# Kernel optimization log

Measured on AMD Instinct MI355X. Metric: run time of the kernel, lower is better.

## Reference

```python
import math
import jax, jax.numpy as jnp
import numpy as np

B, L, H, DH, DV = 4, 4096, 16, 128, 128
CHUNK = 1024
ROPE_BASE = 10000.0


def _rope_tables(length, dim, base, dtype):
    half = dim // 2
    freqs = jnp.exp(jnp.arange(half, dtype=jnp.float32) * (-(math.log(base) / half)))
    angles = jnp.arange(length, dtype=jnp.float32)[:, None] * freqs[None, :]  # (L, half)
    return jnp.cos(angles).astype(dtype), jnp.sin(angles).astype(dtype)


def _apply_rope(x, cos, sin):
    # x: (B, L, H, D); cos/sin: (L, D/2) -> broadcast (1, L, 1, D/2)
    half = x.shape[-1] // 2
    x1, x2 = x[..., :half], x[..., half:]
    c = cos[None, :, None, :]
    s = sin[None, :, None, :]
    return jnp.concatenate([x1 * c - x2 * s, x2 * c + x1 * s], axis=-1)


def setup_inputs() -> dict:
    key = jax.random.key(0)
    kq, kk, kv = jax.random.split(key, 3)
    q = jax.random.normal(kq, (B, L, H, DH), dtype=jnp.float32)
    k = jax.random.normal(kk, (B, L, H, DH), dtype=jnp.float32)
    v = jax.random.normal(kv, (B, L, H, DV), dtype=jnp.float32)
    return {"q": q, "k": k, "v": v}


def reference(q, k, v):
    b, l, h, dh = q.shape
    dv = v.shape[-1]
    n = l // CHUNK  # number of chunks

    cos, sin = _rope_tables(l, dh, ROPE_BASE, q.dtype)
    q = _apply_rope(q, cos, sin)
    k = _apply_rope(k, cos, sin)

    # Chunk-local causal attention: reshape to (B, N, H, C, D)
    qc = q.reshape(b, n, CHUNK, h, dh).transpose(0, 1, 3, 2, 4)
    kc = k.reshape(b, n, CHUNK, h, dh).transpose(0, 1, 3, 2, 4)
    vc = v.reshape(b, n, CHUNK, h, dv).transpose(0, 1, 3, 2, 4)

    scale = 1.0 / math.sqrt(dh)
    scores = jnp.einsum("bnhqd,bnhkd->bnhqk", qc, kc) * scale
    causal = jnp.tril(jnp.ones((CHUNK, CHUNK), dtype=bool))
    scores = jnp.where(causal[None, None, None], scores, jnp.finfo(scores.dtype).min)
    probs = jax.nn.softmax(scores, axis=-1)
    out = jnp.einsum("bnhqk,bnhkd->bnhqd", probs, vc)

    # back to (B, L, H, Dv)
    return out.transpose(0, 1, 3, 2, 4).reshape(b, l, h, dv)
```

## Files before the change

### kernel.cpp

```cpp
#include <hip/hip_runtime.h>
#include <math.h>
#include <stdint.h>


typedef __attribute__((ext_vector_type(8)))  short bf16x8;
typedef __attribute__((ext_vector_type(4)))  short bf16x4;
typedef __attribute__((ext_vector_type(16))) float f32x16;
typedef __attribute__((ext_vector_type(4)))  float f32x4;
typedef __attribute__((ext_vector_type(4)))  unsigned short us4;

__device__ __forceinline__ unsigned short f2bf(float x) {
  unsigned u = __float_as_uint(x);
  u += 0x7fff + ((u >> 16) & 1);
  return (unsigned short)(u >> 16);
}

__global__ __launch_bounds__(256) void rope_kernel(
    const float* __restrict__ q, const float* __restrict__ k,
    unsigned short* __restrict__ qws, unsigned short* __restrict__ kws)
{
  const int w    = threadIdx.x >> 6;
  const int lane = threadIdx.x & 63;
  const int r    = blockIdx.x * 4 + w;
  const int b    = r >> 16;
  const int rem  = r & 65535;
  const int l    = rem >> 4;
  const int h    = rem & 15;
  const float freq  = __builtin_amdgcn_exp2f((float)lane * -0.20762050593046014f);
  const float angle = (float)l * freq;
  float sn, cs;
  sincosf(angle, &sn, &cs);
  const size_t src = (size_t)r * 128 + lane;
  const int n = l >> 10, ck = l & 1023;
  const size_t dst = ((((size_t)b * 4 + n) * 16 + h) * 1024 + ck) * 128 + lane;
  const float QS = 0.12751741f;
  float x1 = q[src], x2 = q[src + 64];
  qws[dst]      = f2bf((x1 * cs - x2 * sn) * QS);
  qws[dst + 64] = f2bf((x2 * cs + x1 * sn) * QS);
  x1 = k[src]; x2 = k[src + 64];
  kws[dst]      = f2bf(x1 * cs - x2 * sn);
  kws[dst + 64] = f2bf(x2 * cs + x1 * sn);
}

__global__ __launch_bounds__(256) void vtrans_kernel(
    const float* __restrict__ v, unsigned short* __restrict__ vtws)
{
  __shared__ unsigned short tile[128 * 72];
  const int t   = threadIdx.x;
  const int ckb = blockIdx.x & 15;
  const int h   = (blockIdx.x >> 4) & 15;
  const int n   = (blockIdx.x >> 8) & 3;
  const int b   = blockIdx.x >> 10;
  const int i0  = (t >> 4) * 4;
  const int dv0 = (t & 15) * 8;
  const int l0  = n * 1024 + ckb * 64;
  const float* src = v + (((size_t)b * 4096 + l0) * 16 + h) * 128;
  unsigned short vals[4][8];
#pragma unroll
  for (int i = 0; i < 4; ++i) {
    const float* p = src + (size_t)(i0 + i) * 2048 + dv0;
    f32x4 a = *(const f32x4*)p;
    f32x4 c = *(const f32x4*)(p + 4);
#pragma unroll
    for (int jj = 0; jj < 4; ++jj) { vals[i][jj] = f2bf(a[jj]); vals[i][4 + jj] = f2bf(c[jj]); }
  }
#pragma unroll
  for (int dd = 0; dd < 8; ++dd) {
    us4 pk = { vals[0][dd], vals[1][dd], vals[2][dd], vals[3][dd] };
    *(us4*)&tile[(dv0 + dd) * 72 + i0] = pk;
  }
  __syncthreads();
  const int dv = t >> 1, hf = t & 1;
  const size_t dstb = ((((size_t)b * 4 + n) * 16 + h) * 128 + dv) * 1024 + ckb * 64 + hf * 32;
  const unsigned short* sl = &tile[dv * 72 + hf * 32];
#pragma unroll
  for (int kk = 0; kk < 4; ++kk)
    *(uint4*)(vtws + dstb + kk * 8) = *(const uint4*)(sl + kk * 8);
}

__global__ __launch_bounds__(256) void attn_kernel(
    const unsigned short* __restrict__ qws, const unsigned short* __restrict__ kws,
    const unsigned short* __restrict__ vtws, float* __restrict__ out)
{
  __shared__ unsigned short smem[64 * 136 + 128 * 72];
  unsigned short* kt = smem;
  unsigned short* vt = smem + 64 * 136;
  unsigned short* qstage = smem;

  const int qt   = blockIdx.x;
  const int nh   = blockIdx.y;
  const int b    = blockIdx.z;
  const int t    = threadIdx.x;
  const int lane = t & 63;
  const int w    = t >> 6;
  const int c    = lane & 31;
  const int g    = lane >> 5;

  const size_t bnh = (size_t)b * 64 + nh;
  const unsigned short* qbase = qws + bnh * (1024 * 128) + (size_t)qt * (128 * 128);
  const unsigned short* kbase = kws + bnh * (1024 * 128);
  const unsigned short* vbase = vtws + bnh * (128 * 1024);

#pragma unroll
  for (int it = 0; it < 8; ++it) {
    int u = it * 256 + t;
    int row = u >> 4, col = u & 15;
    uint4 val = ((const uint4*)qbase)[u];
    *(uint4*)((char*)qstage + row * 272 + col * 16) = val;
  }
  __syncthreads();
  const int qsub = w * 32;
  bf16x8 qf[8];
  {
    const char* qp = (const char*)qstage + (qsub + c) * 272 + g * 16;
#pragma unroll
    for (int f = 0; f < 8; ++f) qf[f] = *(const bf16x8*)(qp + f * 32);
  }
  __syncthreads();

  f32x16 acc[4] = {};
  float m_run = -INFINITY, l_run = 0.0f;
  const int q0w  = qt * 128 + qsub;
  const int rowq = q0w + c;
  const int jmax = 2 * qt + 2;

  for (int j = 0; j < jmax; ++j) {
    const uint4* kg = (const uint4*)(kbase + (size_t)j * (64 * 128));
#pragma unroll
    for (int it = 0; it < 4; ++it) {
      int u = it * 256 + t;
      int row = u >> 4, col = u & 15;
      uint4 val = kg[u];
      *(uint4*)((char*)kt + row * 272 + col * 16) = val;
    }
#pragma unroll
    for (int it = 0; it < 4; ++it) {
      int u = it * 256 + t;
      int dv = u >> 3, col = u & 7;
      uint4 val = *(const uint4*)(vbase + (size_t)dv * 1024 + j * 64 + col * 8);
      *(uint4*)((char*)vt + dv * 144 + col * 16) = val;
    }
    __syncthreads();

    const int kv0 = j * 64;
    if (kv0 <= q0w + 31) {
      f32x16 s[2];
#pragma unroll
      for (int ks = 0; ks < 2; ++ks) {
        f32x16 a = {};
        const char* kp = (const char*)kt + (ks * 32 + c) * 272 + g * 16;
#pragma unroll
        for (int f = 0; f < 8; ++f) {
          bf16x8 kf = *(const bf16x8*)(kp + f * 32);
          a = __builtin_amdgcn_mfma_f32_32x32x16_bf16(kf, qf[f], a, 0, 0, 0);
        }
        s[ks] = a;
      }
      const bool needmask = (kv0 + 63) > q0w;
      float mloc = -INFINITY;
      if (needmask) {
#pragma unroll
        for (int ks = 0; ks < 2; ++ks)
#pragma unroll
          for (int r = 0; r < 16; ++r) {
            int kv = kv0 + ks * 32 + (r & 3) + 8 * (r >> 2) + 4 * g;
            float val = (kv > rowq) ? -3.0e38f : s[ks][r];
            s[ks][r] = val;
            mloc = fmaxf(mloc, val);
          }
      } else {
#pragma unroll
        for (int ks = 0; ks < 2; ++ks)
#pragma unroll
          for (int r = 0; r < 16; ++r) mloc = fmaxf(mloc, s[ks][r]);
      }
      mloc = fmaxf(mloc, __shfl_xor(mloc, 32));
      const float mnew  = fmaxf(m_run, mloc);
      const float alpha = __builtin_amdgcn_exp2f(m_run - mnew);
      float rsum = 0.0f;
#pragma unroll
      for (int ks = 0; ks < 2; ++ks)
#pragma unroll
        for (int r = 0; r < 16; ++r) {
          float p = __builtin_amdgcn_exp2f(s[ks][r] - mnew);
          s[ks][r] = p;
          rsum += p;
        }
      rsum += __shfl_xor(rsum, 32);
      l_run = l_run * alpha + rsum;
      m_run = mnew;
#pragma unroll
      for (int d = 0; d < 4; ++d)
#pragma unroll
        for (int r = 0; r < 16; ++r) acc[d][r] *= alpha;
      bf16x4 pfr[8];
#pragma unroll
      for (int o = 0; o < 8; ++o) {
        const int ks = o >> 2, rb = 4 * (o & 3);
        unsigned u0 = __float_as_uint(s[ks][rb + 0]); u0 += 0x7fff + ((u0 >> 16) & 1);
        unsigned u1 = __float_as_uint(s[ks][rb + 1]); u1 += 0x7fff + ((u1 >> 16) & 1);
        unsigned u2 = __float_as_uint(s[ks][rb + 2]); u2 += 0x7fff + ((u2 >> 16) & 1);
        unsigned u3 = __float_as_uint(s[ks][rb + 3]); u3 += 0x7fff + ((u3 >> 16) & 1);
        union { unsigned uu[2]; bf16x4 bv; } pk;
        pk.uu[0] = __builtin_amdgcn_perm(u1, u0, 0x07060302u);
        pk.uu[1] = __builtin_amdgcn_perm(u3, u2, 0x07060302u);
        pfr[o] = pk.bv;
      }
      const char* vp = (const char*)vt + c * 144 + g * 8;
#pragma unroll
      for (int d = 0; d < 4; ++d) {
        f32x16 a = acc[d];
        const char* vpd = vp + d * 32 * 144;
#pragma unroll
        for (int o = 0; o < 8; ++o) {
          bf16x4 vf = *(const bf16x4*)(vpd + o * 16);
          a = __builtin_amdgcn_mfma_f32_32x32x8bf16_1k(vf, pfr[o], a, 0, 0, 0);
        }
        acc[d] = a;
      }
    }
    __syncthreads();
  }

  const float invl = 1.0f / l_run;
  const int n = nh >> 4, h = nh & 15;
  const size_t orow = (((size_t)b * 4096 + n * 1024 + rowq) * 16 + h) * 128;
#pragma unroll
  for (int d = 0; d < 4; ++d)
#pragma unroll
    for (int e = 0; e < 4; ++e) {
      f32x4 vv;
#pragma unroll
      for (int rr = 0; rr < 4; ++rr) vv[rr] = acc[d][4 * e + rr] * invl;
      *(f32x4*)(out + orow + 32 * d + 8 * e + 4 * g) = vv;
    }
}

extern "C" void kernel_launch(void* const* d_in, const int* in_sizes, int n_in,
                              void* d_out, int out_size, void* d_ws, size_t ws_size,
                              hipStream_t stream) {
  const float* q = (const float*)d_in[0];
  const float* k = (const float*)d_in[1];
  const float* v = (const float*)d_in[2];
  float* out = (float*)d_out;
  unsigned short* qws  = (unsigned short*)d_ws;
  unsigned short* kws  = qws + (size_t)33554432;
  unsigned short* vtws = kws + (size_t)33554432;

  rope_kernel<<<65536, 256, 0, stream>>>(q, k, qws, kws);
  vtrans_kernel<<<4096, 256, 0, stream>>>(v, vtws);
  attn_kernel<<<dim3(8, 64, 4), 256, 0, stream>>>(qws, kws, vtws, out);
}
```

Before: 609.5 us.

## Vectorize RoPE, prefetch K/V tiles into registers, skip redundant rescaling

The RoPE kernel now has each thread handle four elements, using vector loads and stores and hardware sin/cos on range-reduced revolutions instead of sincosf. The attention kernel prefetches the next K/V tile into registers while the current tile is being computed, which overlaps global loads with MFMA work. It also skips the accumulator rescale when no row's max changed, and swaps the grid order so blocks of the same query tile run together. The costs are higher register pressure and slightly lower sin/cos accuracy.

```diff
diff --git a/kernel.cpp b/kernel.cpp
--- a/kernel.cpp
+++ b/kernel.cpp
@@ -19,27 +19,38 @@
     const float* __restrict__ q, const float* __restrict__ k,
     unsigned short* __restrict__ qws, unsigned short* __restrict__ kws)
 {
-  const int w    = threadIdx.x >> 6;
-  const int lane = threadIdx.x & 63;
-  const int r    = blockIdx.x * 4 + w;
-  const int b    = r >> 16;
-  const int rem  = r & 65535;
-  const int l    = rem >> 4;
-  const int h    = rem & 15;
-  const float freq  = __builtin_amdgcn_exp2f((float)lane * -0.20762050593046014f);
-  const float angle = (float)l * freq;
-  float sn, cs;
-  sincosf(angle, &sn, &cs);
-  const size_t src = (size_t)r * 128 + lane;
+  const int t = threadIdx.x;
+  const int r = blockIdx.x * 16 + (t >> 4);
+  const int i = t & 15;
+  const int b = r >> 16;
+  const int l = (r >> 4) & 4095;
+  const int h = r & 15;
+  const size_t src = (size_t)r * 128 + i * 4;
+  const f32x4 q1 = *(const f32x4*)(q + src);
+  const f32x4 q2 = *(const f32x4*)(q + src + 64);
+  const f32x4 k1 = *(const f32x4*)(k + src);
+  const f32x4 k2 = *(const f32x4*)(k + src + 64);
+  const float QS = 0.12751741f;
+  us4 qa, qb, ka, kb;
+#pragma unroll
+  for (int jj = 0; jj < 4; ++jj) {
+    const int j = i * 4 + jj;
+    const float fr  = 0.15915494f * __builtin_amdgcn_exp2f((float)j * -0.20762050593046014f);
+    float rev = (float)l * fr;
+    rev -= floorf(rev);
+    const float sn = __builtin_amdgcn_sinf(rev);
+    const float cs = __builtin_amdgcn_cosf(rev);
+    qa[jj] = f2bf((q1[jj] * cs - q2[jj] * sn) * QS);
+    qb[jj] = f2bf((q2[jj] * cs + q1[jj] * sn) * QS);
+    ka[jj] = f2bf(k1[jj] * cs - k2[jj] * sn);
+    kb[jj] = f2bf(k2[jj] * cs + k1[jj] * sn);
+  }
   const int n = l >> 10, ck = l & 1023;
-  const size_t dst = ((((size_t)b * 4 + n) * 16 + h) * 1024 + ck) * 128 + lane;
-  const float QS = 0.12751741f;
-  float x1 = q[src], x2 = q[src + 64];
-  qws[dst]      = f2bf((x1 * cs - x2 * sn) * QS);
-  qws[dst + 64] = f2bf((x2 * cs + x1 * sn) * QS);
-  x1 = k[src]; x2 = k[src + 64];
-  kws[dst]      = f2bf(x1 * cs - x2 * sn);
-  kws[dst + 64] = f2bf(x2 * cs + x1 * sn);
+  const size_t dst = ((((size_t)b * 4 + n) * 16 + h) * 1024 + ck) * 128 + i * 4;
+  *(us4*)(qws + dst)      = qa;
+  *(us4*)(qws + dst + 64) = qb;
+  *(us4*)(kws + dst)      = ka;
+  *(us4*)(kws + dst + 64) = kb;
 }
 
 __global__ __launch_bounds__(256) void vtrans_kernel(
@@ -87,8 +98,8 @@
   unsigned short* vt = smem + 64 * 136;
   unsigned short* qstage = smem;
 
-  const int qt   = blockIdx.x;
-  const int nh   = blockIdx.y;
+  const int nh   = blockIdx.x;
+  const int qt   = blockIdx.y;
   const int b    = blockIdx.z;
   const int t    = threadIdx.x;
   const int lane = t & 63;
@@ -101,6 +112,18 @@
   const unsigned short* kbase = kws + bnh * (1024 * 128);
   const unsigned short* vbase = vtws + bnh * (128 * 1024);
 
+  uint4 kpre[4], vpre[4];
+  {
+    const uint4* kg = (const uint4*)kbase;
+#pragma unroll
+    for (int it = 0; it < 4; ++it) kpre[it] = kg[it * 256 + t];
+#pragma unroll
+    for (int it = 0; it < 4; ++it) {
+      int dv = it * 32 + (t >> 3);
+      vpre[it] = *(const uint4*)(vbase + (size_t)dv * 1024 + (t & 7) * 8);
+    }
+  }
+
 #pragma unroll
   for (int it = 0; it < 8; ++it) {
     int u = it * 256 + t;
@@ -116,7 +139,6 @@
 #pragma unroll
     for (int f = 0; f < 8; ++f) qf[f] = *(const bf16x8*)(qp + f * 32);
   }
-  __syncthreads();
 
   f32x16 acc[4] = {};
   float m_run = -INFINITY, l_run = 0.0f;
@@ -125,22 +147,29 @@
   const int jmax = 2 * qt + 2;
 
   for (int j = 0; j < jmax; ++j) {
-    const uint4* kg = (const uint4*)(kbase + (size_t)j * (64 * 128));
+    __syncthreads();
 #pragma unroll
     for (int it = 0; it < 4; ++it) {
-      int u = it * 256 + t;
-      int row = u >> 4, col = u & 15;
-      uint4 val = kg[u];
-      *(uint4*)((char*)kt + row * 272 + col * 16) = val;
+      int row = it * 16 + (t >> 4);
+      *(uint4*)((char*)kt + row * 272 + (t & 15) * 16) = kpre[it];
     }
 #pragma unroll
     for (int it = 0; it < 4; ++it) {
-      int u = it * 256 + t;
-      int dv = u >> 3, col = u & 7;
-      uint4 val = *(const uint4*)(vbase + (size_t)dv * 1024 + j * 64 + col * 8);
-      *(uint4*)((char*)vt + dv * 144 + col * 16) = val;
+      int dv = it * 32 + (t >> 3);
+      *(uint4*)((char*)vt + dv * 144 + (t & 7) * 16) = vpre[it];
     }
     __syncthreads();
+    if (j + 1 < jmax) {
+      const uint4* kg = (const uint4*)(kbase + (size_t)(j + 1) * (64 * 128));
+#pragma unroll
+      for (int it = 0; it < 4; ++it) kpre[it] = kg[it * 256 + t];
+      const unsigned short* vg = vbase + (size_t)(j + 1) * 64;
+#pragma unroll
+      for (int it = 0; it < 4; ++it) {
+        int dv = it * 32 + (t >> 3);
+        vpre[it] = *(const uint4*)(vg + (size_t)dv * 1024 + (t & 7) * 8);
+      }
+    }
 
     const int kv0 = j * 64;
     if (kv0 <= q0w + 31) {
@@ -175,8 +204,16 @@
           for (int r = 0; r < 16; ++r) mloc = fmaxf(mloc, s[ks][r]);
       }
       mloc = fmaxf(mloc, __shfl_xor(mloc, 32));
-      const float mnew  = fmaxf(m_run, mloc);
-      const float alpha = __builtin_amdgcn_exp2f(m_run - mnew);
+      const float mnew = fmaxf(m_run, mloc);
+      if (__any(mloc > m_run)) {
+        const float alpha = __builtin_amdgcn_exp2f(m_run - mnew);
+        l_run *= alpha;
+#pragma unroll
+        for (int d = 0; d < 4; ++d)
+#pragma unroll
+          for (int r = 0; r < 16; ++r) acc[d][r] *= alpha;
+      }
+      m_run = mnew;
       float rsum = 0.0f;
 #pragma unroll
       for (int ks = 0; ks < 2; ++ks)
@@ -187,12 +224,7 @@
           rsum += p;
         }
       rsum += __shfl_xor(rsum, 32);
-      l_run = l_run * alpha + rsum;
-      m_run = mnew;
-#pragma unroll
-      for (int d = 0; d < 4; ++d)
-#pragma unroll
-        for (int r = 0; r < 16; ++r) acc[d][r] *= alpha;
+      l_run += rsum;
       bf16x4 pfr[8];
 #pragma unroll
       for (int o = 0; o < 8; ++o) {
@@ -219,7 +251,6 @@
         acc[d] = a;
       }
     }
-    __syncthreads();
   }
 
   const float invl = 1.0f / l_run;
@@ -247,7 +278,7 @@
   unsigned short* kws  = qws + (size_t)33554432;
   unsigned short* vtws = kws + (size_t)33554432;
 
-  rope_kernel<<<65536, 256, 0, stream>>>(q, k, qws, kws);
+  rope_kernel<<<16384, 256, 0, stream>>>(q, k, qws, kws);
   vtrans_kernel<<<4096, 256, 0, stream>>>(v, vtws);
-  attn_kernel<<<dim3(8, 64, 4), 256, 0, stream>>>(qws, kws, vtws, out);
-}
+  attn_kernel<<<dim3(64, 8, 4), 256, 0, stream>>>(qws, kws, vtws, out);
+}
```

Measured after the change: 692.8 us. +13.7%, slower.
